# Kernel tuning notes

Measured on AMD Instinct MI355X. Metric: run time of the kernel, lower is better.

The kernel has to match this reference:

```python
import jax, jax.numpy as jnp
import numpy as np

SEQ = 2048
DIM = 512
HEADS = 8
DH = DIM // HEADS
EPS = float(np.finfo(np.float32).eps)
NEG = float(np.finfo(np.float32).max)


def _pos_encoding(seq, dim):
    idx = jnp.arange(seq, dtype=jnp.float32)
    div = 1.0 / (10000.0 ** (jnp.arange(0, dim, 2, dtype=jnp.float32) / dim) + EPS)
    ang = idx[:, None] * div[None, :]  # [S, dim/2]
    pos = jnp.zeros((seq, dim), dtype=jnp.float32)
    pos = pos.at[:, 0::2].set(jnp.sin(ang)).at[:, 1::2].set(jnp.cos(ang))
    return pos[None]  # [1, S, D]


def _rmsnorm(x, gain, bias):
    d = x.shape[-1]
    scale = jnp.linalg.norm(x, axis=-1, keepdims=True) * (d ** -0.5)
    return x / (scale + EPS) * gain + bias


def setup_inputs() -> dict:
    key = jax.random.key(0)
    ks = jax.random.split(key, 12)
    s = 0.02
    return {
        "x": jax.random.normal(ks[0], (4, SEQ, DIM), dtype=jnp.float32),
        "norm1_g": jnp.ones((DIM,), jnp.float32),
        "norm1_b": jnp.zeros((DIM,), jnp.float32),
        "wq": jax.random.normal(ks[1], (DIM, DIM), jnp.float32) * s,
        "wk": jax.random.normal(ks[2], (DIM, DIM), jnp.float32) * s,
        "wv": jax.random.normal(ks[3], (DIM, DIM), jnp.float32) * s,
        "wo": jax.random.normal(ks[4], (DIM, DIM), jnp.float32) * s,
        "norm2_g": jnp.ones((DIM,), jnp.float32),
        "norm2_b": jnp.zeros((DIM,), jnp.float32),
        "ff_w1": jax.random.normal(ks[5], (DIM, DIM), jnp.float32) * s,
        "ff_b1": jnp.zeros((DIM,), jnp.float32),
        "ffn_g": jnp.ones((DIM,), jnp.float32),
        "ffn_b": jnp.zeros((DIM,), jnp.float32),
        "sw_w": jax.random.normal(ks[6], (2 * DIM, DIM), jnp.float32) * s,
        "sw_b": jnp.zeros((2 * DIM,), jnp.float32),
        "ff_w2": jax.random.normal(ks[7], (DIM, DIM), jnp.float32) * s,
        "ff_b2": jnp.zeros((DIM,), jnp.float32),
    }


def _block(x, norm1_g, norm1_b, wq, wk, wv, wo, norm2_g, norm2_b,
           ff_w1, ff_b1, ffn_g, ffn_b, sw_w, sw_b, ff_w2, ff_b2):
    B = x.shape[0]
    x = x + _pos_encoding(SEQ, DIM)

    # --- multi-head attention on RMSNorm(x) ---
    h = _rmsnorm(x, norm1_g, norm1_b)
    q = (h @ wq.T).reshape(B, SEQ, HEADS, DH).transpose(0, 2, 1, 3)  # [B,H,S,Dh]
    k = (h @ wk.T).reshape(B, SEQ, HEADS, DH).transpose(0, 2, 1, 3)
    v = (h @ wv.T).reshape(B, SEQ, HEADS, DH).transpose(0, 2, 1, 3)
    scores = jnp.einsum("bhqd,bhkd->bhqk", q, k)  # materialized [B,H,S,S]
    causal_mask = jnp.triu(jnp.ones((SEQ, SEQ), dtype=bool), k=1)
    scores = jnp.where(causal_mask[None, None], -NEG, scores)
    # NOTE: original scales by dim_k**-0.5 = dim_emb**-0.5 (not head dim)
    attn = jax.nn.softmax(scores * (DIM ** -0.5), axis=-1)
    o = jnp.einsum("bhqk,bhkd->bhqd", attn, v)
    o = o.transpose(0, 2, 1, 3).reshape(B, SEQ, DIM) @ wo.T
    x = x + o

    # --- feed-forward: Linear -> RMSNorm -> SwiGLU -> Linear ---
    h = _rmsnorm(x, norm2_g, norm2_b)
    h = h @ ff_w1.T + ff_b1
    h = _rmsnorm(h, ffn_g, ffn_b)
    u = h @ sw_w.T + sw_b  # [B,S,2*DIM]
    h = jax.nn.silu(u[..., :DIM]) + u[..., DIM:]
    h = h @ ff_w2.T + ff_b2
    return x + h


def reference(x, norm1_g, norm1_b, wq, wk, wv, wo, norm2_g, norm2_b,
              ff_w1, ff_b1, ffn_g, ffn_b, sw_w, sw_b, ff_w2, ff_b2):
    return _block(x, norm1_g, norm1_b, wq, wk, wv, wo, norm2_g, norm2_b,
                  ff_w1, ff_b1, ffn_g, ffn_b, sw_w, sw_b, ff_w2, ff_b2)
```

## Files before the change

kernel.cpp:

```cpp
#include <hip/hip_runtime.h>
#include <hip/hip_bf16.h>
#include <cstdint>
#include <cstddef>

typedef __bf16 bf16;
typedef __bf16 bf16x4_t __attribute__((ext_vector_type(4)));
typedef __bf16 bf16x8_t __attribute__((ext_vector_type(8)));
typedef float f32x4 __attribute__((ext_vector_type(4)));
typedef float f32x16 __attribute__((ext_vector_type(16)));

#define DEV_INLINE __device__ __forceinline__

constexpr int SEQ = 2048, DIM = 512, HEADS = 8, DH = 64;
constexpr int ROWS = 4 * SEQ;
constexpr float EPSF = 1.1920928955078125e-07f;
constexpr float RSQRT_DIM = 0.04419417382415922f;
constexpr float LOG2E = 1.44269504088896f;

DEV_INLINE void load_lds16(const void* g, void* l) {
  __builtin_amdgcn_global_load_lds(
      (const __attribute__((address_space(1))) void*)g,
      (__attribute__((address_space(3))) void*)l,
      16, 0, 0);
}

DEV_INLINE unsigned int packbf(float a, float b) {
  union { unsigned int u; bf16 h[2]; } z;
  z.h[0] = (bf16)a;
  z.h[1] = (bf16)b;
  return z.u;
}

DEV_INLINE void permswap(unsigned int& a, unsigned int& b) {
  asm volatile("v_permlane32_swap_b32 %0, %1" : "+v"(a), "+v"(b));
}

__global__ __launch_bounds__(256) void cvt_all_k(
    const float* __restrict__ wq, const float* __restrict__ wk,
    const float* __restrict__ wv, const float* __restrict__ wo,
    const float* __restrict__ w1, const float* __restrict__ sww,
    const float* __restrict__ w2, bf16* __restrict__ dst) {
  const int i = blockIdx.x * 256 + threadIdx.x;
  const float* src;
  int local;
  if (i < 196608)      { src = (i < 65536) ? wq : (i < 131072) ? wk : wv; local = i & 65535; }
  else if (i < 262144) { src = wo;  local = i - 196608; }
  else if (i < 327680) { src = w1;  local = i - 262144; }
  else if (i < 458752) { src = sww; local = i - 327680; }
  else                 { src = w2;  local = i - 458752; }
  float4 f = reinterpret_cast<const float4*>(src)[local];
  bf16x4_t o;
  o[0] = (bf16)f.x; o[1] = (bf16)f.y; o[2] = (bf16)f.z; o[3] = (bf16)f.w;
  reinterpret_cast<bf16x4_t*>(dst)[i] = o;
}

template <bool ADDPOS>
__global__ __launch_bounds__(256) void rmsnorm_k(const float* __restrict__ in,
                                                 const float* __restrict__ gain,
                                                 const float* __restrict__ bias,
                                                 float* __restrict__ outF,
                                                 bf16* __restrict__ outB) {
  const int sub = threadIdx.x >> 7;
  const int row = blockIdx.x * 2 + sub;
  const int t = threadIdx.x & 127;
  const float* rp = in + (size_t)row * DIM;
  float4 v = reinterpret_cast<const float4*>(rp)[t];
  if constexpr (ADDPOS) {
    const int s = row & (SEQ - 1);
    const float e0 = (float)(4 * t) * (1.0f / (float)DIM);
    const float e1 = (float)(4 * t + 2) * (1.0f / (float)DIM);
    const float d0 = 1.0f / (powf(10000.0f, e0) + EPSF);
    const float d1 = 1.0f / (powf(10000.0f, e1) + EPSF);
    const float a0 = (float)s * d0, a1 = (float)s * d1;
    v.x += sinf(a0); v.y += cosf(a0);
    v.z += sinf(a1); v.w += cosf(a1);
  }
  float ss = v.x * v.x + v.y * v.y + v.z * v.z + v.w * v.w;
#pragma unroll
  for (int off = 32; off > 0; off >>= 1) ss += __shfl_down(ss, off, 64);
  __shared__ float red[4];
  const int wv = threadIdx.x >> 6;
  if ((threadIdx.x & 63) == 0) red[wv] = ss;
  __syncthreads();
  const float total = red[sub * 2] + red[sub * 2 + 1];
  const float scale = sqrtf(total) * RSQRT_DIM;
  const float inv = 1.0f / (scale + EPSF);
  if constexpr (ADDPOS)
    reinterpret_cast<float4*>(outF + (size_t)row * DIM)[t] = v;
  const float4 g = reinterpret_cast<const float4*>(gain)[t];
  const float4 bb = reinterpret_cast<const float4*>(bias)[t];
  bf16x4_t o;
  o[0] = (bf16)(v.x * inv * g.x + bb.x);
  o[1] = (bf16)(v.y * inv * g.y + bb.y);
  o[2] = (bf16)(v.z * inv * g.z + bb.z);
  o[3] = (bf16)(v.w * inv * g.w + bb.w);
  reinterpret_cast<bf16x4_t*>(outB + (size_t)row * DIM)[t] = o;
}

enum { MODE_QKV = 0, MODE_RES = 1, MODE_BIAS = 2, MODE_SWIGLU2 = 3, MODE_RESBIAS = 4 };

template <int MODE>
__global__ __launch_bounds__(256) void gemm_bt_k(
    const bf16* __restrict__ A, const bf16* __restrict__ Bt,
    const float* __restrict__ bias, const float* __restrict__ res,
    float* __restrict__ outF, bf16* __restrict__ outB,
    bf16* __restrict__ oq, bf16* __restrict__ okk, bf16* __restrict__ ovT) {
  constexpr int NST = (MODE == MODE_SWIGLU2) ? 2 : 3;
  constexpr int BELEMS = (MODE == MODE_SWIGLU2) ? 8192 : 4096;
  __shared__ __align__(16) bf16 sA[NST][128 * 64];
  __shared__ __align__(16) bf16 sB[NST][BELEMS];
  const int tid = threadIdx.x;
  const int wave = tid >> 6, lane = tid & 63;
  const int m0 = blockIdx.x * 128, n0 = blockIdx.y * 64;
  const int wm = wave >> 1, wn = wave & 1;
  const int lr = lane & 15, hi4 = lane >> 4;
  const int xw = lr & 7;

  const f32x4 fzero = {0.f, 0.f, 0.f, 0.f};
  f32x4 acc[4][2], acc2[4][2];
#pragma unroll
  for (int i = 0; i < 4; ++i)
#pragma unroll
    for (int j = 0; j < 2; ++j) { acc[i][j] = fzero; acc2[i][j] = fzero; }

  const int rowt = tid >> 3, slot = tid & 7;
  const int sxor = (slot ^ (rowt & 7)) << 4;

  auto stage = [&](int buf, int kt) {
    const size_t k0b = (size_t)kt * 128;
#pragma unroll
    for (int c = 0; c < 4; ++c) {
      const int row = c * 32 + rowt;
      load_lds16((const char*)A + (size_t)(m0 + row) * 1024 + k0b + sxor,
                 (char*)&sA[buf][0] + c * 4096 + tid * 16);
    }
#pragma unroll
    for (int c = 0; c < 2; ++c) {
      const int row = c * 32 + rowt;
      load_lds16((const char*)Bt + (size_t)(n0 + row) * 1024 + k0b + sxor,
                 (char*)&sB[buf][0] + c * 4096 + tid * 16);
    }
    if constexpr (MODE == MODE_SWIGLU2) {
#pragma unroll
      for (int c = 0; c < 2; ++c) {
        const int row = c * 32 + rowt;
        load_lds16((const char*)Bt + (size_t)(512 + n0 + row) * 1024 + k0b + sxor,
                   (char*)&sB[buf][0] + 8192 + c * 4096 + tid * 16);
      }
    }
  };

  if constexpr (NST == 3) {
    stage(0, 0);
    stage(1, 1);
    asm volatile("s_waitcnt vmcnt(6)\ns_barrier" ::: "memory");
  } else {
    stage(0, 0);
    asm volatile("s_waitcnt vmcnt(0)\ns_barrier" ::: "memory");
  }

#pragma unroll
  for (int kt = 0; kt < 8; ++kt) {
    const int cur = kt % NST;
    if constexpr (NST == 3) {
      if (kt + 2 < 8) stage((kt + 2) % 3, kt + 2);
    } else {
      if (kt + 1 < 8) stage((kt + 1) & 1, kt + 1);
    }
    const char* sa = (const char*)&sA[cur][0];
    const char* sb = (const char*)&sB[cur][0];
#pragma unroll
    for (int ks = 0; ks < 2; ++ks) {
      const int so = ((ks * 4 + hi4) ^ xw) << 4;
      bf16x8_t af[4], bfr[2], bfr2[2];
#pragma unroll
      for (int mf = 0; mf < 4; ++mf)
        af[mf] = *(const bf16x8_t*)(sa + (wm * 64 + mf * 16 + lr) * 128 + so);
#pragma unroll
      for (int nf = 0; nf < 2; ++nf) {
        bfr[nf] = *(const bf16x8_t*)(sb + (wn * 32 + nf * 16 + lr) * 128 + so);
        if constexpr (MODE == MODE_SWIGLU2)
          bfr2[nf] = *(const bf16x8_t*)(sb + 8192 + (wn * 32 + nf * 16 + lr) * 128 + so);
      }
#pragma unroll
      for (int mf = 0; mf < 4; ++mf)
#pragma unroll
        for (int nf = 0; nf < 2; ++nf) {
          acc[mf][nf] = __builtin_amdgcn_mfma_f32_16x16x32_bf16(af[mf], bfr[nf],
                                                                acc[mf][nf], 0, 0, 0);
          if constexpr (MODE == MODE_SWIGLU2)
            acc2[mf][nf] = __builtin_amdgcn_mfma_f32_16x16x32_bf16(af[mf], bfr2[nf],
                                                                   acc2[mf][nf], 0, 0, 0);
        }
    }
    if constexpr (NST == 3) {
      if (kt + 2 < 8)
        asm volatile("s_waitcnt vmcnt(6)\ns_barrier" ::: "memory");
      else if (kt + 1 < 8)
        asm volatile("s_waitcnt vmcnt(0)\ns_barrier" ::: "memory");
    } else {
      if (kt + 1 < 8)
        asm volatile("s_waitcnt vmcnt(0)\ns_barrier" ::: "memory");
    }
  }

  if constexpr (MODE == MODE_QKV) {
    const int which = n0 >> 9;
    const int h = (n0 >> 6) & 7;
    const int b = m0 >> 11;
    const int s0tok = m0 & 2047;
    bf16* st = &sA[0][0];
    const int rb = wm * 64 + hi4 * 4;
    const int cb = wn * 32 + lr;
    __syncthreads();
    if (which < 2) {
#pragma unroll
      for (int mf = 0; mf < 4; ++mf)
#pragma unroll
        for (int nf = 0; nf < 2; ++nf)
#pragma unroll
          for (int rg = 0; rg < 4; ++rg) {
            float v = acc[mf][nf][rg];
            if (which == 0) v *= RSQRT_DIM * LOG2E;
            st[(rb + mf * 16 + rg) * 72 + cb + nf * 16] = (bf16)v;
          }
      __syncthreads();
      bf16* dst = which == 0 ? oq : okk;
#pragma unroll
      for (int j = 0; j < 4; ++j) {
        const int flat = j * 4096 + tid * 16;
        const int row = flat >> 7, offb = flat & 127;
        bf16x8_t vv = *(const bf16x8_t*)(st + row * 72 + offb / 2);
        const size_t addr =
            ((size_t)((b * HEADS + h) * SEQ + s0tok + row)) * DH + offb / 2;
        *(bf16x8_t*)(dst + addr) = vv;
      }
    } else {
#pragma unroll
      for (int mf = 0; mf < 4; ++mf)
#pragma unroll
        for (int nf = 0; nf < 2; ++nf)
#pragma unroll
          for (int rg = 0; rg < 4; ++rg)
            st[(cb + nf * 16) * 136 + rb + mf * 16 + rg] = (bf16)acc[mf][nf][rg];
      __syncthreads();
#pragma unroll
      for (int j = 0; j < 4; ++j) {
        const int flat = j * 4096 + tid * 16;
        const int row = flat >> 8, offb = flat & 255;
        bf16x8_t vv = *(const bf16x8_t*)(st + row * 136 + offb / 2);
        const size_t addr =
            ((size_t)((b * HEADS + h) * DH + row)) * SEQ + s0tok + offb / 2;
        *(bf16x8_t*)(ovT + addr) = vv;
      }
    }
    return;
  }

  const int rbase = m0 + wm * 64 + hi4 * 4;
  const int cbase = n0 + wn * 32 + lr;
#pragma unroll
  for (int mf = 0; mf < 4; ++mf) {
#pragma unroll
    for (int nf = 0; nf < 2; ++nf) {
      const int c = cbase + nf * 16;
#pragma unroll
      for (int rg = 0; rg < 4; ++rg) {
        const int r = rbase + mf * 16 + rg;
        float v = acc[mf][nf][rg];
        if constexpr (MODE == MODE_RES) {
          const size_t idx = (size_t)r * 512 + c;
          outF[idx] = res[idx] + v;
        } else if constexpr (MODE == MODE_BIAS) {
          const size_t idx = (size_t)r * 512 + c;
          outF[idx] = v + bias[c];
        } else if constexpr (MODE == MODE_SWIGLU2) {
          const size_t idx = (size_t)r * 512 + c;
          const float u1 = v + bias[c];
          const float u2 = acc2[mf][nf][rg] + bias[512 + c];
          const float sig = 1.0f / (1.0f + __expf(-u1));
          outB[idx] = (bf16)(u1 * sig + u2);
        } else {
          const size_t idx = (size_t)r * 512 + c;
          outF[idx] = res[idx] + v + bias[c];
        }
      }
    }
  }
}

__constant__ int kSlot[24] = {
  7 | 0,  15 | 16, 15 | 32, 14 | 16, 14 | 32, 6 | 0,  13 | 16, 13 | 32,
  12 | 16, 12 | 32, 5 | 0,  11 | 16, 11 | 32, 10 | 16, 10 | 32, 4 | 0,
  9 | 16, 9 | 32,  8 | 16,  8 | 32,  3 | 0,  2 | 0,  1 | 0,  0 | 0};

__global__ __launch_bounds__(256)
__attribute__((amdgpu_waves_per_eu(2)))
void attn_k(const bf16* __restrict__ Q,
            const bf16* __restrict__ K,
            const bf16* __restrict__ VT,
            bf16* __restrict__ O,
            float* __restrict__ scrO,
            float* __restrict__ scrL) {
  const int tid = threadIdx.x;
  const int wave = tid >> 6, lane = tid & 63;
  const int lq = lane & 31, hi = lane >> 5;

  const int wg = blockIdx.x;
  const int xcd = wg & 7;
  const int bh = xcd * 4 + ((wg >> 3) & 3);
  const int enc = kSlot[wg >> 5];
  const int qi = enc & 15;
  const int mode = enc >> 4;
  const int qw = qi * 128 + wave * 32;
  const int kt0 = (mode == 2) ? (qi + 1) : 0;
  const int ktEnd = (mode == 1) ? (qi + 1) : (2 * qi + 2);
  const int nkt = (mode == 1) ? ktEnd : (2 * qi + 1 + (wave >> 1));

  const char* Kg = (const char*)(K + (size_t)bh * SEQ * DH);
  const char* Vg = (const char*)(VT + (size_t)bh * DH * SEQ);
  const bf16* Qp = Q + (size_t)bh * SEQ * DH;

  __shared__ __align__(16) bf16 smem[6][4096];

  bf16x8_t qf[4];
  {
    const bf16* qp = Qp + (size_t)(qw + lq) * DH + 8 * hi;
    qf[0] = *(const bf16x8_t*)(qp);
    qf[1] = *(const bf16x8_t*)(qp + 16);
    qf[2] = *(const bf16x8_t*)(qp + 32);
    qf[3] = *(const bf16x8_t*)(qp + 48);
  }

  bf16x8_t ones;
#pragma unroll
  for (int i = 0; i < 8; ++i) ones[i] = (bf16)1.0f;

  const int slot = lane & 7, rsub = lane >> 3;
  const int sgoff = (slot * 16) ^ (rsub << 4);

  auto stage = [&](int buf, int kt) {
#pragma unroll
    for (int c = 0; c < 2; ++c) {
      const int row = c * 32 + wave * 8 + rsub;
      const int ldsb = c * 4096 + wave * 1024 + lane * 16;
      load_lds16(Kg + (size_t)(kt * 64 + row) * 128 + sgoff,
                 (char*)&smem[buf][0] + ldsb);
      load_lds16(Vg + (size_t)row * 4096 + (size_t)kt * 128 + sgoff,
                 (char*)&smem[3 + buf][0] + ldsb);
    }
  };

  stage(0, kt0);
  stage(1, kt0 + 1);
  asm volatile("s_waitcnt vmcnt(4)\ns_barrier" ::: "memory");

  f32x16 oa0, oa1, ls;
#pragma unroll
  for (int r = 0; r < 16; ++r) { oa0[r] = 0.f; oa1[r] = 0.f; ls[r] = 0.f; }
  const int xorv = (lq & 7) << 4;

  union U8 { unsigned int u[4]; bf16x8_t v; };

  for (int kt = kt0; kt < ktEnd; ++kt) {
    const int rel = kt - kt0;
    const int buf = rel % 3;
    if (kt + 2 < ktEnd) stage((rel + 2) % 3, kt + 2);
    if (kt < nkt) {
      const char* kb = (const char*)&smem[buf][0];
      const char* vb = (const char*)&smem[3 + buf][0];

      f32x16 s0, s1;
#pragma unroll
      for (int r = 0; r < 16; ++r) { s0[r] = 0.f; s1[r] = 0.f; }
      __builtin_amdgcn_s_setprio(1);
#pragma unroll
      for (int s = 0; s < 4; ++s) {
        const int bo = (32 * s + 16 * hi) ^ xorv;
        s0 = __builtin_amdgcn_mfma_f32_32x32x16_bf16(
            *(const bf16x8_t*)(kb + lq * 128 + bo), qf[s], s0, 0, 0, 0);
        s1 = __builtin_amdgcn_mfma_f32_32x32x16_bf16(
            *(const bf16x8_t*)(kb + (32 + lq) * 128 + bo), qf[s], s1, 0, 0, 0);
      }
      __builtin_amdgcn_s_setprio(0);
      asm volatile("" : "+v"(s0), "+v"(s1));

      if (mode != 1 && kt == nkt - 1) {
        const int qg = qw + lq;
#pragma unroll
        for (int r = 0; r < 16; ++r) {
          const int kl = kt * 64 + (r & 3) + 8 * (r >> 2) + 4 * hi;
          if (kl > qg) s0[r] = -3.0e38f;
          if (kl + 32 > qg) s1[r] = -3.0e38f;
        }
      }

#pragma unroll
      for (int r = 0; r < 16; ++r) {
        s0[r] = exp2f(s0[r]);
        s1[r] = exp2f(s1[r]);
      }

      U8 p00, p01, p10, p11;
      {
        unsigned int x0, x1, y0, y1;
        x0 = packbf(s0[0], s0[1]);  x1 = packbf(s0[4], s0[5]);
        y0 = packbf(s0[2], s0[3]);  y1 = packbf(s0[6], s0[7]);
        permswap(x0, x1); permswap(y0, y1);
        p00.u[0] = x0; p00.u[2] = x1; p00.u[1] = y0; p00.u[3] = y1;
        x0 = packbf(s0[8], s0[9]);   x1 = packbf(s0[12], s0[13]);
        y0 = packbf(s0[10], s0[11]); y1 = packbf(s0[14], s0[15]);
        permswap(x0, x1); permswap(y0, y1);
        p01.u[0] = x0; p01.u[2] = x1; p01.u[1] = y0; p01.u[3] = y1;
        x0 = packbf(s1[0], s1[1]);  x1 = packbf(s1[4], s1[5]);
        y0 = packbf(s1[2], s1[3]);  y1 = packbf(s1[6], s1[7]);
        permswap(x0, x1); permswap(y0, y1);
        p10.u[0] = x0; p10.u[2] = x1; p10.u[1] = y0; p10.u[3] = y1;
        x0 = packbf(s1[8], s1[9]);   x1 = packbf(s1[12], s1[13]);
        y0 = packbf(s1[10], s1[11]); y1 = packbf(s1[14], s1[15]);
        permswap(x0, x1); permswap(y0, y1);
        p11.u[0] = x0; p11.u[2] = x1; p11.u[1] = y0; p11.u[3] = y1;
      }

      ls = __builtin_amdgcn_mfma_f32_32x32x16_bf16(ones, p00.v, ls, 0, 0, 0);
      ls = __builtin_amdgcn_mfma_f32_32x32x16_bf16(ones, p01.v, ls, 0, 0, 0);
      ls = __builtin_amdgcn_mfma_f32_32x32x16_bf16(ones, p10.v, ls, 0, 0, 0);
      ls = __builtin_amdgcn_mfma_f32_32x32x16_bf16(ones, p11.v, ls, 0, 0, 0);

      __builtin_amdgcn_s_setprio(1);
      {
        const int b0 = (16 * hi) ^ xorv;
        const int b1 = (32 + 16 * hi) ^ xorv;
        const int b2 = (64 + 16 * hi) ^ xorv;
        const int b3 = (96 + 16 * hi) ^ xorv;
        oa0 = __builtin_amdgcn_mfma_f32_32x32x16_bf16(
            *(const bf16x8_t*)(vb + lq * 128 + b0), p00.v, oa0, 0, 0, 0);
        oa0 = __builtin_amdgcn_mfma_f32_32x32x16_bf16(
            *(const bf16x8_t*)(vb + lq * 128 + b1), p01.v, oa0, 0, 0, 0);
        oa0 = __builtin_amdgcn_mfma_f32_32x32x16_bf16(
            *(const bf16x8_t*)(vb + lq * 128 + b2), p10.v, oa0, 0, 0, 0);
        oa0 = __builtin_amdgcn_mfma_f32_32x32x16_bf16(
            *(const bf16x8_t*)(vb + lq * 128 + b3), p11.v, oa0, 0, 0, 0);
        oa1 = __builtin_amdgcn_mfma_f32_32x32x16_bf16(
            *(const bf16x8_t*)(vb + (32 + lq) * 128 + b0), p00.v, oa1, 0, 0, 0);
        oa1 = __builtin_amdgcn_mfma_f32_32x32x16_bf16(
            *(const bf16x8_t*)(vb + (32 + lq) * 128 + b1), p01.v, oa1, 0, 0, 0);
        oa1 = __builtin_amdgcn_mfma_f32_32x32x16_bf16(
            *(const bf16x8_t*)(vb + (32 + lq) * 128 + b2), p10.v, oa1, 0, 0, 0);
        oa1 = __builtin_amdgcn_mfma_f32_32x32x16_bf16(
            *(const bf16x8_t*)(vb + (32 + lq) * 128 + b3), p11.v, oa1, 0, 0, 0);
      }
      __builtin_amdgcn_s_setprio(0);
    }
    if (kt + 2 < ktEnd)
      asm volatile("s_waitcnt vmcnt(4)\ns_barrier" ::: "memory");
    else
      asm volatile("s_waitcnt vmcnt(0)\ns_barrier" ::: "memory");
  }

  if (mode == 0) {
    const float inv = 1.0f / ls[0];
    bf16* ol = &smem[0][0] + wave * 2560;
#pragma unroll
    for (int t4 = 0; t4 < 4; ++t4) {
      const int d0 = 8 * t4 + 4 * hi;
      *(unsigned int*)(ol + lq * 80 + d0)          = packbf(oa0[4 * t4] * inv, oa0[4 * t4 + 1] * inv);
      *(unsigned int*)(ol + lq * 80 + d0 + 2)      = packbf(oa0[4 * t4 + 2] * inv, oa0[4 * t4 + 3] * inv);
      *(unsigned int*)(ol + lq * 80 + 32 + d0)     = packbf(oa1[4 * t4] * inv, oa1[4 * t4 + 1] * inv);
      *(unsigned int*)(ol + lq * 80 + 32 + d0 + 2) = packbf(oa1[4 * t4 + 2] * inv, oa1[4 * t4 + 3] * inv);
    }
    const int b = bh >> 3, h = bh & 7;
#pragma unroll
    for (int ps = 0; ps < 4; ++ps) {
      const int flat = ps * 1024 + lane * 16;
      const int qr = flat >> 7, off = flat & 127;
      bf16x8_t vv = *(const bf16x8_t*)((const char*)ol + qr * 160 + off);
      *(bf16x8_t*)(O + ((size_t)(b * SEQ + qw + qr)) * DIM + h * 64 + off / 2) = vv;
    }
  } else {
    const float lrow = ls[0];
    float* so = scrO + ((size_t)(mode - 1) * 256 + bh * 8 + (qi - 8)) * 8192;
    const int qoff = (wave * 32 + lq) * 64;
#pragma unroll
    for (int t4 = 0; t4 < 4; ++t4) {
      const int d0 = 8 * t4 + 4 * hi;
      f32x4 w0 = {oa0[4 * t4], oa0[4 * t4 + 1], oa0[4 * t4 + 2], oa0[4 * t4 + 3]};
      f32x4 w1 = {oa1[4 * t4], oa1[4 * t4 + 1], oa1[4 * t4 + 2], oa1[4 * t4 + 3]};
      *(f32x4*)(so + qoff + d0) = w0;
      *(f32x4*)(so + qoff + 32 + d0) = w1;
    }
    if (!hi)
      scrL[(mode - 1) * 32768 + bh * 1024 + (qi - 8) * 128 + wave * 32 + lq] = lrow;
  }
}

__global__ __launch_bounds__(256) void attn_merge_k(
    const float* __restrict__ scrO, const float* __restrict__ scrL,
    bf16* __restrict__ O) {
  const int i = blockIdx.x * 256 + threadIdx.x;
  const int bh = i >> 14;
  const int rem = i & 16383;
  const int u = rem >> 4;
  const int dq = (rem & 15) << 2;
  const size_t oA = ((size_t)bh * 8 + (u >> 7)) * 8192 + (u & 127) * 64 + dq;
  const f32x4 a = *(const f32x4*)(scrO + oA);
  const f32x4 b = *(const f32x4*)(scrO + 2097152 + oA);
  const float l = scrL[bh * 1024 + u] + scrL[32768 + bh * 1024 + u];
  const float inv = 1.0f / l;
  const int bb = bh >> 3, h = bh & 7;
  bf16x4_t o;
  o[0] = (bf16)((a[0] + b[0]) * inv);
  o[1] = (bf16)((a[1] + b[1]) * inv);
  o[2] = (bf16)((a[2] + b[2]) * inv);
  o[3] = (bf16)((a[3] + b[3]) * inv);
  *(bf16x4_t*)(O + ((size_t)(bb * SEQ + 1024 + u)) * DIM + h * 64 + dq) = o;
}

extern "C" void kernel_launch(void* const* d_in, const int* in_sizes, int n_in,
                              void* d_out, int out_size, void* d_ws, size_t ws_size,
                              hipStream_t stream) {
  const float* x   = (const float*)d_in[0];
  const float* n1g = (const float*)d_in[1];
  const float* n1b = (const float*)d_in[2];
  const float* wq  = (const float*)d_in[3];
  const float* wk  = (const float*)d_in[4];
  const float* wv  = (const float*)d_in[5];
  const float* wo  = (const float*)d_in[6];
  const float* n2g = (const float*)d_in[7];
  const float* n2b = (const float*)d_in[8];
  const float* w1  = (const float*)d_in[9];
  const float* b1  = (const float*)d_in[10];
  const float* ffg = (const float*)d_in[11];
  const float* ffb = (const float*)d_in[12];
  const float* sww = (const float*)d_in[13];
  const float* swb = (const float*)d_in[14];
  const float* w2  = (const float*)d_in[15];
  const float* b2  = (const float*)d_in[16];
  float* out = (float*)d_out;

  char* ws = (char*)d_ws;
  float* x1 = (float*)(ws + 0);
  float* x2 = (float*)(ws + 16777216);
  bf16* hbuf   = (bf16*)(ws + 33554432);
  bf16* qbuf   = (bf16*)(ws + 41943040);
  bf16* kbuf   = (bf16*)(ws + 50331648);
  bf16* vtbuf  = (bf16*)(ws + 58720256);
  bf16* obuf   = (bf16*)(ws + 67108864);
  bf16* wbase  = (bf16*)(ws + 75497472);
  bf16* wqkv_b = wbase;
  bf16* wo_b   = wbase + 786432;
  bf16* w1_b   = wbase + 1048576;
  bf16* sw_b16 = wbase + 1310720;
  bf16* w2_b   = wbase + 1835008;
  float* scrO  = (float*)x2;
  float* scrL  = (float*)hbuf;

  cvt_all_k<<<2048, 256, 0, stream>>>(wq, wk, wv, wo, w1, sww, w2, wbase);

  rmsnorm_k<true><<<ROWS / 2, 256, 0, stream>>>(x, n1g, n1b, x1, hbuf);

  gemm_bt_k<MODE_QKV><<<dim3(64, 24), 256, 0, stream>>>(
      hbuf, wqkv_b, nullptr, nullptr, nullptr, nullptr, qbuf, kbuf, vtbuf);

  attn_k<<<768, 256, 0, stream>>>(qbuf, kbuf, vtbuf, obuf, scrO, scrL);
  attn_merge_k<<<2048, 256, 0, stream>>>(scrO, scrL, obuf);

  gemm_bt_k<MODE_RES><<<dim3(64, 8), 256, 0, stream>>>(
      obuf, wo_b, nullptr, x1, x2, nullptr, nullptr, nullptr, nullptr);

  rmsnorm_k<false><<<ROWS / 2, 256, 0, stream>>>(x2, n2g, n2b, nullptr, hbuf);

  gemm_bt_k<MODE_BIAS><<<dim3(64, 8), 256, 0, stream>>>(
      hbuf, w1_b, b1, nullptr, x1, nullptr, nullptr, nullptr, nullptr);

  rmsnorm_k<false><<<ROWS / 2, 256, 0, stream>>>(x1, ffg, ffb, nullptr, hbuf);

  gemm_bt_k<MODE_SWIGLU2><<<dim3(64, 8), 256, 0, stream>>>(
      hbuf, sw_b16, swb, nullptr, nullptr, qbuf, nullptr, nullptr, nullptr);

  gemm_bt_k<MODE_RESBIAS><<<dim3(64, 8), 256, 0, stream>>>(
      qbuf, w2_b, b2, x2, out, nullptr, nullptr, nullptr, nullptr);
}
```

Baseline: 149.5 us.

## Store residual stream in bf16 and fuse split-attention merge into attn kernel

Residual intermediates x1/x2 and the FFN hidden output become bf16 instead of fp32, halving their write and read traffic across the residual GEMMs and RMSNorms. The separate attn_merge kernel is removed: the two split-KV halves for each query tile coordinate through an atomic counter, and whichever finishes second reads the partner's partial output and normaliser, combines them, and writes the final bf16 output. This saves a launch and a pass over scratch memory but adds a memset, threadfences and an atomic. The residual path now carries bf16 rounding, lowering accuracy.

```diff
diff --git a/kernel.cpp b/kernel.cpp
--- a/kernel.cpp
+++ b/kernel.cpp
@@ -54,17 +54,23 @@
   reinterpret_cast<bf16x4_t*>(dst)[i] = o;
 }
 
-template <bool ADDPOS>
-__global__ __launch_bounds__(256) void rmsnorm_k(const float* __restrict__ in,
+template <bool ADDPOS, bool INBF>
+__global__ __launch_bounds__(256) void rmsnorm_k(const void* __restrict__ in,
                                                  const float* __restrict__ gain,
                                                  const float* __restrict__ bias,
-                                                 float* __restrict__ outF,
+                                                 bf16* __restrict__ outR,
                                                  bf16* __restrict__ outB) {
   const int sub = threadIdx.x >> 7;
   const int row = blockIdx.x * 2 + sub;
   const int t = threadIdx.x & 127;
-  const float* rp = in + (size_t)row * DIM;
-  float4 v = reinterpret_cast<const float4*>(rp)[t];
+  float4 v;
+  if constexpr (INBF) {
+    bf16x4_t b4 = reinterpret_cast<const bf16x4_t*>(
+        (const bf16*)in + (size_t)row * DIM)[t];
+    v.x = (float)b4[0]; v.y = (float)b4[1]; v.z = (float)b4[2]; v.w = (float)b4[3];
+  } else {
+    v = reinterpret_cast<const float4*>((const float*)in + (size_t)row * DIM)[t];
+  }
   if constexpr (ADDPOS) {
     const int s = row & (SEQ - 1);
     const float e0 = (float)(4 * t) * (1.0f / (float)DIM);
@@ -85,8 +91,11 @@
   const float total = red[sub * 2] + red[sub * 2 + 1];
   const float scale = sqrtf(total) * RSQRT_DIM;
   const float inv = 1.0f / (scale + EPSF);
-  if constexpr (ADDPOS)
-    reinterpret_cast<float4*>(outF + (size_t)row * DIM)[t] = v;
+  if constexpr (ADDPOS) {
+    bf16x4_t r4;
+    r4[0] = (bf16)v.x; r4[1] = (bf16)v.y; r4[2] = (bf16)v.z; r4[3] = (bf16)v.w;
+    reinterpret_cast<bf16x4_t*>(outR + (size_t)row * DIM)[t] = r4;
+  }
   const float4 g = reinterpret_cast<const float4*>(gain)[t];
   const float4 bb = reinterpret_cast<const float4*>(bias)[t];
   bf16x4_t o;
@@ -102,7 +111,7 @@
 template <int MODE>
 __global__ __launch_bounds__(256) void gemm_bt_k(
     const bf16* __restrict__ A, const bf16* __restrict__ Bt,
-    const float* __restrict__ bias, const float* __restrict__ res,
+    const float* __restrict__ bias, const bf16* __restrict__ resB,
     float* __restrict__ outF, bf16* __restrict__ outB,
     bf16* __restrict__ oq, bf16* __restrict__ okk, bf16* __restrict__ ovT) {
   constexpr int NST = (MODE == MODE_SWIGLU2) ? 2 : 3;
@@ -268,21 +277,18 @@
       for (int rg = 0; rg < 4; ++rg) {
         const int r = rbase + mf * 16 + rg;
         float v = acc[mf][nf][rg];
+        const size_t idx2 = (size_t)r * 512 + c;
         if constexpr (MODE == MODE_RES) {
-          const size_t idx = (size_t)r * 512 + c;
-          outF[idx] = res[idx] + v;
+          outB[idx2] = (bf16)((float)resB[idx2] + v);
         } else if constexpr (MODE == MODE_BIAS) {
-          const size_t idx = (size_t)r * 512 + c;
-          outF[idx] = v + bias[c];
+          outB[idx2] = (bf16)(v + bias[c]);
         } else if constexpr (MODE == MODE_SWIGLU2) {
-          const size_t idx = (size_t)r * 512 + c;
           const float u1 = v + bias[c];
           const float u2 = acc2[mf][nf][rg] + bias[512 + c];
           const float sig = 1.0f / (1.0f + __expf(-u1));
-          outB[idx] = (bf16)(u1 * sig + u2);
+          outB[idx2] = (bf16)(u1 * sig + u2);
         } else {
-          const size_t idx = (size_t)r * 512 + c;
-          outF[idx] = res[idx] + v + bias[c];
+          outF[idx2] = (float)resB[idx2] + v + bias[c];
         }
       }
     }
@@ -301,10 +307,12 @@
             const bf16* __restrict__ VT,
             bf16* __restrict__ O,
             float* __restrict__ scrO,
-            float* __restrict__ scrL) {
+            float* __restrict__ scrL,
+            int* __restrict__ flags) {
   const int tid = threadIdx.x;
   const int wave = tid >> 6, lane = tid & 63;
   const int lq = lane & 31, hi = lane >> 5;
+  __shared__ int second;
 
   const int wg = blockIdx.x;
   const int xcd = wg & 7;
@@ -458,28 +466,12 @@
       asm volatile("s_waitcnt vmcnt(0)\ns_barrier" ::: "memory");
   }
 
+  float inv;
   if (mode == 0) {
-    const float inv = 1.0f / ls[0];
-    bf16* ol = &smem[0][0] + wave * 2560;
-#pragma unroll
-    for (int t4 = 0; t4 < 4; ++t4) {
-      const int d0 = 8 * t4 + 4 * hi;
-      *(unsigned int*)(ol + lq * 80 + d0)          = packbf(oa0[4 * t4] * inv, oa0[4 * t4 + 1] * inv);
-      *(unsigned int*)(ol + lq * 80 + d0 + 2)      = packbf(oa0[4 * t4 + 2] * inv, oa0[4 * t4 + 3] * inv);
-      *(unsigned int*)(ol + lq * 80 + 32 + d0)     = packbf(oa1[4 * t4] * inv, oa1[4 * t4 + 1] * inv);
-      *(unsigned int*)(ol + lq * 80 + 32 + d0 + 2) = packbf(oa1[4 * t4 + 2] * inv, oa1[4 * t4 + 3] * inv);
-    }
-    const int b = bh >> 3, h = bh & 7;
-#pragma unroll
-    for (int ps = 0; ps < 4; ++ps) {
-      const int flat = ps * 1024 + lane * 16;
-      const int qr = flat >> 7, off = flat & 127;
-      bf16x8_t vv = *(const bf16x8_t*)((const char*)ol + qr * 160 + off);
-      *(bf16x8_t*)(O + ((size_t)(b * SEQ + qw + qr)) * DIM + h * 64 + off / 2) = vv;
-    }
+    inv = 1.0f / ls[0];
   } else {
-    const float lrow = ls[0];
-    float* so = scrO + ((size_t)(mode - 1) * 256 + bh * 8 + (qi - 8)) * 8192;
+    const int pidx = bh * 8 + (qi - 8);
+    float* so = scrO + ((size_t)(mode - 1) * 256 + pidx) * 8192;
     const int qoff = (wave * 32 + lq) * 64;
 #pragma unroll
     for (int t4 = 0; t4 < 4; ++t4) {
@@ -489,31 +481,46 @@
       *(f32x4*)(so + qoff + d0) = w0;
       *(f32x4*)(so + qoff + 32 + d0) = w1;
     }
-    if (!hi)
-      scrL[(mode - 1) * 32768 + bh * 1024 + (qi - 8) * 128 + wave * 32 + lq] = lrow;
-  }
-}
-
-__global__ __launch_bounds__(256) void attn_merge_k(
-    const float* __restrict__ scrO, const float* __restrict__ scrL,
-    bf16* __restrict__ O) {
-  const int i = blockIdx.x * 256 + threadIdx.x;
-  const int bh = i >> 14;
-  const int rem = i & 16383;
-  const int u = rem >> 4;
-  const int dq = (rem & 15) << 2;
-  const size_t oA = ((size_t)bh * 8 + (u >> 7)) * 8192 + (u & 127) * 64 + dq;
-  const f32x4 a = *(const f32x4*)(scrO + oA);
-  const f32x4 b = *(const f32x4*)(scrO + 2097152 + oA);
-  const float l = scrL[bh * 1024 + u] + scrL[32768 + bh * 1024 + u];
-  const float inv = 1.0f / l;
-  const int bb = bh >> 3, h = bh & 7;
-  bf16x4_t o;
-  o[0] = (bf16)((a[0] + b[0]) * inv);
-  o[1] = (bf16)((a[1] + b[1]) * inv);
-  o[2] = (bf16)((a[2] + b[2]) * inv);
-  o[3] = (bf16)((a[3] + b[3]) * inv);
-  *(bf16x4_t*)(O + ((size_t)(bb * SEQ + 1024 + u)) * DIM + h * 64 + dq) = o;
+    const int lidx = bh * 1024 + (qi - 8) * 128 + wave * 32 + lq;
+    if (!hi) scrL[(mode - 1) * 32768 + lidx] = ls[0];
+    __threadfence();
+    if (tid == 0) second = atomicAdd(&flags[pidx], 1);
+    __syncthreads();
+    if (second == 0) return;
+    __threadfence();
+    const int om = 3 - mode;
+    const float* soo = scrO + ((size_t)(om - 1) * 256 + pidx) * 8192;
+    const float lo = scrL[(om - 1) * 32768 + lidx];
+    inv = 1.0f / (ls[0] + lo);
+#pragma unroll
+    for (int t4 = 0; t4 < 4; ++t4) {
+      const int d0 = 8 * t4 + 4 * hi;
+      f32x4 q0 = *(const f32x4*)(soo + qoff + d0);
+      f32x4 q1 = *(const f32x4*)(soo + qoff + 32 + d0);
+      oa0[4 * t4] += q0[0];     oa0[4 * t4 + 1] += q0[1];
+      oa0[4 * t4 + 2] += q0[2]; oa0[4 * t4 + 3] += q0[3];
+      oa1[4 * t4] += q1[0];     oa1[4 * t4 + 1] += q1[1];
+      oa1[4 * t4 + 2] += q1[2]; oa1[4 * t4 + 3] += q1[3];
+    }
+  }
+
+  bf16* ol = &smem[0][0] + wave * 2560;
+#pragma unroll
+  for (int t4 = 0; t4 < 4; ++t4) {
+    const int d0 = 8 * t4 + 4 * hi;
+    *(unsigned int*)(ol + lq * 80 + d0)          = packbf(oa0[4 * t4] * inv, oa0[4 * t4 + 1] * inv);
+    *(unsigned int*)(ol + lq * 80 + d0 + 2)      = packbf(oa0[4 * t4 + 2] * inv, oa0[4 * t4 + 3] * inv);
+    *(unsigned int*)(ol + lq * 80 + 32 + d0)     = packbf(oa1[4 * t4] * inv, oa1[4 * t4 + 1] * inv);
+    *(unsigned int*)(ol + lq * 80 + 32 + d0 + 2) = packbf(oa1[4 * t4 + 2] * inv, oa1[4 * t4 + 3] * inv);
+  }
+  const int b = bh >> 3, h = bh & 7;
+#pragma unroll
+  for (int ps = 0; ps < 4; ++ps) {
+    const int flat = ps * 1024 + lane * 16;
+    const int qr = flat >> 7, off = flat & 127;
+    bf16x8_t vv = *(const bf16x8_t*)((const char*)ol + qr * 160 + off);
+    *(bf16x8_t*)(O + ((size_t)(b * SEQ + qw + qr)) * DIM + h * 64 + off / 2) = vv;
+  }
 }
 
 extern "C" void kernel_launch(void* const* d_in, const int* in_sizes, int n_in,
@@ -539,45 +546,46 @@
   float* out = (float*)d_out;
 
   char* ws = (char*)d_ws;
-  float* x1 = (float*)(ws + 0);
-  float* x2 = (float*)(ws + 16777216);
-  bf16* hbuf   = (bf16*)(ws + 33554432);
-  bf16* qbuf   = (bf16*)(ws + 41943040);
-  bf16* kbuf   = (bf16*)(ws + 50331648);
-  bf16* vtbuf  = (bf16*)(ws + 58720256);
-  bf16* obuf   = (bf16*)(ws + 67108864);
-  bf16* wbase  = (bf16*)(ws + 75497472);
+  bf16* x1b   = (bf16*)(ws + 0);
+  bf16* x2b   = (bf16*)(ws + 8388608);
+  float* scrO = (float*)(ws + 16777216);
+  bf16* hbuf  = (bf16*)(ws + 33554432);
+  float* scrL = (float*)hbuf;
+  int*  flags = (int*)(ws + 33554432 + 262144);
+  bf16* qbuf  = (bf16*)(ws + 41943040);
+  bf16* kbuf  = (bf16*)(ws + 50331648);
+  bf16* vtbuf = (bf16*)(ws + 58720256);
+  bf16* obuf  = (bf16*)(ws + 67108864);
+  bf16* wbase = (bf16*)(ws + 75497472);
   bf16* wqkv_b = wbase;
   bf16* wo_b   = wbase + 786432;
   bf16* w1_b   = wbase + 1048576;
   bf16* sw_b16 = wbase + 1310720;
   bf16* w2_b   = wbase + 1835008;
-  float* scrO  = (float*)x2;
-  float* scrL  = (float*)hbuf;
 
   cvt_all_k<<<2048, 256, 0, stream>>>(wq, wk, wv, wo, w1, sww, w2, wbase);
 
-  rmsnorm_k<true><<<ROWS / 2, 256, 0, stream>>>(x, n1g, n1b, x1, hbuf);
+  rmsnorm_k<true, false><<<ROWS / 2, 256, 0, stream>>>(x, n1g, n1b, x1b, hbuf);
 
   gemm_bt_k<MODE_QKV><<<dim3(64, 24), 256, 0, stream>>>(
       hbuf, wqkv_b, nullptr, nullptr, nullptr, nullptr, qbuf, kbuf, vtbuf);
 
-  attn_k<<<768, 256, 0, stream>>>(qbuf, kbuf, vtbuf, obuf, scrO, scrL);
-  attn_merge_k<<<2048, 256, 0, stream>>>(scrO, scrL, obuf);
+  hipMemsetAsync(flags, 0, 1024, stream);
+  attn_k<<<768, 256, 0, stream>>>(qbuf, kbuf, vtbuf, obuf, scrO, scrL, flags);
 
   gemm_bt_k<MODE_RES><<<dim3(64, 8), 256, 0, stream>>>(
-      obuf, wo_b, nullptr, x1, x2, nullptr, nullptr, nullptr, nullptr);
-
-  rmsnorm_k<false><<<ROWS / 2, 256, 0, stream>>>(x2, n2g, n2b, nullptr, hbuf);
+      obuf, wo_b, nullptr, x1b, nullptr, x2b, nullptr, nullptr, nullptr);
+
+  rmsnorm_k<false, true><<<ROWS / 2, 256, 0, stream>>>(x2b, n2g, n2b, nullptr, hbuf);
 
   gemm_bt_k<MODE_BIAS><<<dim3(64, 8), 256, 0, stream>>>(
-      hbuf, w1_b, b1, nullptr, x1, nullptr, nullptr, nullptr, nullptr);
-
-  rmsnorm_k<false><<<ROWS / 2, 256, 0, stream>>>(x1, ffg, ffb, nullptr, hbuf);
+      hbuf, w1_b, b1, nullptr, nullptr, x1b, nullptr, nullptr, nullptr);
+
+  rmsnorm_k<false, true><<<ROWS / 2, 256, 0, stream>>>(x1b, ffg, ffb, nullptr, hbuf);
 
   gemm_bt_k<MODE_SWIGLU2><<<dim3(64, 8), 256, 0, stream>>>(
       hbuf, sw_b16, swb, nullptr, nullptr, qbuf, nullptr, nullptr, nullptr);
 
   gemm_bt_k<MODE_RESBIAS><<<dim3(64, 8), 256, 0, stream>>>(
-      qbuf, w2_b, b2, x2, out, nullptr, nullptr, nullptr, nullptr);
-}
+      qbuf, w2_b, b2, x2b, out, nullptr, nullptr, nullptr, nullptr);
+}
```

Result: slower. 238.7 us (+59.6%).
